# Kernel optimization log

Measured on AMD Instinct MI355X. Metric: run time of the kernel, lower is better.

The kernel has to match this reference:

```python
import jax, jax.numpy as jnp
import numpy as np

HEADS = 8
DIM_HEAD = 32
SCALE = DIM_HEAD ** (-0.5)


def setup_inputs() -> dict:
    key = jax.random.key(0)
    k1, k2, k3 = jax.random.split(key, 3)
    b, c, d, h, w = 4, 128, 32, 32, 32
    hidden = HEADS * DIM_HEAD  # 256
    x = jax.random.normal(k1, (b, c, d, h, w), dtype=jnp.float32)
    # 1x1x1 convs are channel GEMMs; store kernels as [out, in]
    w_qkv = jax.random.normal(k2, (3 * hidden, c), dtype=jnp.float32) * (1.0 / np.sqrt(c))
    w_out = jax.random.normal(k3, (c, hidden), dtype=jnp.float32) * (1.0 / np.sqrt(hidden))
    b_out = jnp.zeros((c,), dtype=jnp.float32)
    return {"x": x, "w_qkv": w_qkv, "w_out": w_out, "b_out": b_out}


def reference(x, w_qkv, w_out, b_out):
    b, c, d, h, w = x.shape
    n = d * h * w
    xf = x.reshape(b, c, n)  # [b, c, n]
    qkv = jnp.einsum('oc,bcn->bon', w_qkv, xf)  # [b, 3*hidden, n]
    q, k, v = jnp.split(qkv, 3, axis=1)
    # [b, heads, dim_head, n]
    q = q.reshape(b, HEADS, DIM_HEAD, n)
    k = k.reshape(b, HEADS, DIM_HEAD, n)
    v = v.reshape(b, HEADS, DIM_HEAD, n)
    q = jax.nn.softmax(q, axis=-2) * SCALE  # softmax over feature dim
    k = jax.nn.softmax(k, axis=-1)          # softmax over sequence dim
    context = jnp.einsum('bhdn,bhen->bhde', k, v)  # [b,h,d,e]
    out = jnp.einsum('bhde,bhdn->bhen', context, q)  # [b,h,e,n]
    out = out.reshape(b, HEADS * DIM_HEAD, n)
    out = jnp.einsum('oc,bcn->bon', w_out, out) + b_out[None, :, None]
    return out.reshape(b, c, d, h, w)
```

## Files before the change

### kernel.cpp

```cpp
#include <hip/hip_runtime.h>
#include <hip/hip_bf16.h>

#define CC 128
#define NN 32768
#define QSCALE 0.17677669529663687f

typedef unsigned short ushort_t;
typedef __attribute__((ext_vector_type(8))) short bf16x8;
typedef __attribute__((ext_vector_type(4))) short short4v;
typedef __attribute__((ext_vector_type(4))) float f32x4;

#define U_WQB    0
#define U_WKVB   32768
#define U_MFOLD  98304
#define F_PART   114688
#define F_PACC   4440064
#define F_SACC   4472832

#define XPITCH 136
#define KVP 72
#define QPITCH 264

__device__ __forceinline__ ushort_t f2b(float f) {
    __hip_bfloat16 h = __float2bfloat16(f);
    return *reinterpret_cast<ushort_t*>(&h);
}
__device__ __forceinline__ float b2f(ushort_t u) {
    union { unsigned u32; float f; } cv; cv.u32 = (unsigned)u << 16; return cv.f;
}
__device__ __forceinline__ f32x4 mfma16(bf16x8 a, bf16x8 b, f32x4 c) {
    return __builtin_amdgcn_mfma_f32_16x16x32_bf16(a, b, c, 0, 0, 0);
}

__global__ void prep_kernel(const float* __restrict__ wqkv, ushort_t* __restrict__ wsb,
                            float* __restrict__ Pacc, float* __restrict__ sacc) {
    int idx = blockIdx.x * 256 + threadIdx.x;
    if (idx < 32768) {
        wsb[U_WQB + idx] = f2b(wqkv[idx]);
        Pacc[idx] = 0.f;
        if (idx < 1024) sacc[idx] = 0.f;
    } else {
        int i2 = idx - 32768;
        int p = i2 >> 15, r = (i2 >> 7) & 255, c = i2 & 127;
        int hh = r >> 6, t = (r >> 5) & 1, d = r & 31;
        int src = 256 + t * 256 + (p * 4 + hh) * 32 + d;
        wsb[U_WKVB + i2] = f2b(wqkv[src * 128 + c]);
    }
}

__global__ __launch_bounds__(512, 4) void kv_context_kernel(
        const float* __restrict__ x, const ushort_t* __restrict__ wkvb,
        float* __restrict__ part) {
    __shared__ ushort_t u_lds[8 * 64 * KVP];
    int blk = blockIdx.x;
    int b = blk >> 7, win = blk & 127;
    int tid = threadIdx.x;
    int lane = tid & 63, wv = tid >> 6;
    int l16 = lane & 15, quad = lane >> 4;

    f32x4 accP[2][2];
    #pragma unroll
    for (int i = 0; i < 2; ++i)
        #pragma unroll
        for (int j = 0; j < 2; ++j) accP[i][j] = (f32x4){0.f, 0.f, 0.f, 0.f};
    float accSl0 = 0.f, accSl1 = 0.f;

    ushort_t* x_lds = u_lds;
    ushort_t* kvw = u_lds + wv * (64 * KVP);
    int ct = tid >> 4;
    int n4v = (tid & 15) * 4;
    int c0 = ct * 4;
    const float* xb = x + ((size_t)(b * 128 + c0)) * NN;
    const ushort_t* wbase = wkvb + wv * (64 * 128);

    #pragma unroll 1
    for (int ch = 0; ch < 4; ++ch) {
        int n0 = win * 256 + ch * 64;
        float4 r0 = *(const float4*)(xb + 0 * (size_t)NN + n0 + n4v);
        float4 r1 = *(const float4*)(xb + 1 * (size_t)NN + n0 + n4v);
        float4 r2 = *(const float4*)(xb + 2 * (size_t)NN + n0 + n4v);
        float4 r3 = *(const float4*)(xb + 3 * (size_t)NN + n0 + n4v);
        { short4v pk; pk[0]=(short)f2b(r0.x); pk[1]=(short)f2b(r1.x); pk[2]=(short)f2b(r2.x); pk[3]=(short)f2b(r3.x);
          *(short4v*)&x_lds[(n4v + 0) * XPITCH + c0] = pk; }
        { short4v pk; pk[0]=(short)f2b(r0.y); pk[1]=(short)f2b(r1.y); pk[2]=(short)f2b(r2.y); pk[3]=(short)f2b(r3.y);
          *(short4v*)&x_lds[(n4v + 1) * XPITCH + c0] = pk; }
        { short4v pk; pk[0]=(short)f2b(r0.z); pk[1]=(short)f2b(r1.z); pk[2]=(short)f2b(r2.z); pk[3]=(short)f2b(r3.z);
          *(short4v*)&x_lds[(n4v + 2) * XPITCH + c0] = pk; }
        { short4v pk; pk[0]=(short)f2b(r0.w); pk[1]=(short)f2b(r1.w); pk[2]=(short)f2b(r2.w); pk[3]=(short)f2b(r3.w);
          *(short4v*)&x_lds[(n4v + 3) * XPITCH + c0] = pk; }
        __syncthreads();
        bf16x8 xf[4][4];
        #pragma unroll
        for (int s = 0; s < 4; ++s)
            #pragma unroll
            for (int k = 0; k < 4; ++k)
                xf[s][k] = *(const bf16x8*)&x_lds[(s * 16 + l16) * XPITCH + k * 32 + quad * 8];
        __syncthreads();
        #pragma unroll
        for (int T = 0; T < 4; ++T) {
            f32x4 a0 = (f32x4){0.f,0.f,0.f,0.f}, a1 = a0, a2 = a0, a3 = a0;
            #pragma unroll
            for (int k = 0; k < 4; ++k) {
                bf16x8 wfk = *(const bf16x8*)&wbase[(T * 16 + l16) * 128 + k * 32 + quad * 8];
                a0 = mfma16(xf[0][k], wfk, a0);
                a1 = mfma16(xf[1][k], wfk, a1);
                a2 = mfma16(xf[2][k], wfk, a2);
                a3 = mfma16(xf[3][k], wfk, a3);
            }
            #pragma unroll
            for (int s = 0; s < 4; ++s) {
                f32x4 a = (s == 0) ? a0 : (s == 1) ? a1 : (s == 2) ? a2 : a3;
                short4v pk;
                if (T < 2) {
                    #pragma unroll
                    for (int r = 0; r < 4; ++r) pk[r] = (short)f2b(__expf(a[r]));
                    float es = b2f((ushort_t)pk[0]) + b2f((ushort_t)pk[1])
                             + b2f((ushort_t)pk[2]) + b2f((ushort_t)pk[3]);
                    if (T == 0) accSl0 += es; else accSl1 += es;
                } else {
                    #pragma unroll
                    for (int r = 0; r < 4; ++r) pk[r] = (short)f2b(a[r]);
                }
                *(short4v*)&kvw[(T * 16 + l16) * KVP + s * 16 + quad * 4] = pk;
            }
        }
        #pragma unroll
        for (int k2 = 0; k2 < 2; ++k2) {
            int noff = k2 * 32 + quad * 8;
            bf16x8 ea0 = *(const bf16x8*)&kvw[(0 * 16 + l16) * KVP + noff];
            bf16x8 ea1 = *(const bf16x8*)&kvw[(1 * 16 + l16) * KVP + noff];
            bf16x8 vb0 = *(const bf16x8*)&kvw[(32 + 0 * 16 + l16) * KVP + noff];
            bf16x8 vb1 = *(const bf16x8*)&kvw[(32 + 1 * 16 + l16) * KVP + noff];
            accP[0][0] = mfma16(ea0, vb0, accP[0][0]);
            accP[0][1] = mfma16(ea0, vb1, accP[0][1]);
            accP[1][0] = mfma16(ea1, vb0, accP[1][0]);
            accP[1][1] = mfma16(ea1, vb1, accP[1][1]);
        }
        __syncthreads();
    }
    float s0 = accSl0; s0 += __shfl_xor(s0, 16); s0 += __shfl_xor(s0, 32);
    float s1 = accSl1; s1 += __shfl_xor(s1, 16); s1 += __shfl_xor(s1, 32);
    float* ph = part + (size_t)blk * 8448 + wv * 1056;
    #pragma unroll
    for (int i = 0; i < 2; ++i)
        #pragma unroll
        for (int j = 0; j < 2; ++j)
            #pragma unroll
            for (int r = 0; r < 4; ++r)
                ph[(i * 16 + quad * 4 + r) * 32 + j * 16 + l16] = accP[i][j][r];
    if (quad == 0) {
        ph[1024 + l16] = s0;
        ph[1024 + 16 + l16] = s1;
    }
}

__global__ void reduce_kernel(const float* __restrict__ part,
                              float* __restrict__ Pacc, float* __restrict__ sacc) {
    int q = blockIdx.x / 132;
    int idx = (blockIdx.x - q * 132) * 256 + threadIdx.x;
    if (idx >= 32 * 1056) return;
    int bh = idx / 1056, pos = idx - bh * 1056;
    int b = bh >> 3, h = bh & 7;
    const float* pb = part + (size_t)b * 128 * 8448 + (size_t)q * 32 * 8448 + h * 1056 + pos;
    float a = 0.f;
    #pragma unroll 8
    for (int wnd = 0; wnd < 32; ++wnd)
        a += pb[(size_t)wnd * 8448];
    if (pos < 1024) atomicAdd(Pacc + (size_t)bh * 1024 + pos, a);
    else            atomicAdd(sacc + bh * 32 + (pos - 1024), a);
}

__global__ void context_proj_kernel(const float* __restrict__ wout,
                                    const float* __restrict__ Pacc,
                                    const float* __restrict__ sacc,
                                    ushort_t* __restrict__ mfold) {
    int blk = blockIdx.x;
    int b = blk >> 7, cout = blk & 127;
    int hd = threadIdx.x;
    int h = hd >> 5, d = hd & 31;
    int bh = b * 8 + h;
    float inv = 1.0f / sacc[bh * 32 + d];
    const float* Pr = Pacc + (size_t)bh * 1024 + d * 32;
    const float* wr = wout + cout * 256 + h * 32;
    float a = 0.f;
    #pragma unroll
    for (int e = 0; e < 32; ++e) a += wr[e] * Pr[e];
    mfold[((size_t)(b * 128 + cout)) * 256 + hd] = f2b(a * inv);
}

__global__ __launch_bounds__(256, 3) void q_out_kernel(
        const float* __restrict__ x, const ushort_t* __restrict__ wqb,
        const ushort_t* __restrict__ mfold, const float* __restrict__ bout,
        float* __restrict__ out) {
    __shared__ ushort_t x_lds[64 * XPITCH];
    __shared__ ushort_t qs_lds[64 * QPITCH];
    int blk = blockIdx.x;
    int b = blk >> 9, tile = blk & 511;
    int n0 = tile * 64;
    int tid = threadIdx.x;
    int lane = tid & 63, wv = tid >> 6;
    int l16 = lane & 15, quad = lane >> 4;

    const ushort_t* wq = wqb + ((wv * 64 + l16) * 128) + quad * 8;

    {
        int ct = tid >> 4, n4v = (tid & 15) * 4;
        #pragma unroll
        for (int i = 0; i < 2; ++i) {
            int c0 = i * 64 + ct * 4;
            const float* xb = x + ((size_t)(b * 128 + c0)) * NN + n0 + n4v;
            float4 r0 = *(const float4*)(xb + 0 * (size_t)NN);
            float4 r1 = *(const float4*)(xb + 1 * (size_t)NN);
            float4 r2 = *(const float4*)(xb + 2 * (size_t)NN);
            float4 r3 = *(const float4*)(xb + 3 * (size_t)NN);
            { short4v pk; pk[0]=(short)f2b(r0.x); pk[1]=(short)f2b(r1.x); pk[2]=(short)f2b(r2.x); pk[3]=(short)f2b(r3.x);
              *(short4v*)&x_lds[(n4v + 0) * XPITCH + c0] = pk; }
            { short4v pk; pk[0]=(short)f2b(r0.y); pk[1]=(short)f2b(r1.y); pk[2]=(short)f2b(r2.y); pk[3]=(short)f2b(r3.y);
              *(short4v*)&x_lds[(n4v + 1) * XPITCH + c0] = pk; }
            { short4v pk; pk[0]=(short)f2b(r0.z); pk[1]=(short)f2b(r1.z); pk[2]=(short)f2b(r2.z); pk[3]=(short)f2b(r3.z);
              *(short4v*)&x_lds[(n4v + 2) * XPITCH + c0] = pk; }
            { short4v pk; pk[0]=(short)f2b(r0.w); pk[1]=(short)f2b(r1.w); pk[2]=(short)f2b(r2.w); pk[3]=(short)f2b(r3.w);
              *(short4v*)&x_lds[(n4v + 3) * XPITCH + c0] = pk; }
        }
    }
    bf16x8 afA[4], afB[4];
    #pragma unroll
    for (int mt = 0; mt < 4; ++mt)
        afA[mt] = *(const bf16x8*)&wq[mt * 2048];
    __syncthreads();

    f32x4 acc[4][4];
    #pragma unroll
    for (int mt = 0; mt < 4; ++mt)
        #pragma unroll
        for (int nt = 0; nt < 4; ++nt) acc[mt][nt] = (f32x4){0.f, 0.f, 0.f, 0.f};
    #pragma unroll
    for (int k = 0; k < 4; ++k) {
        if (k < 3) {
            #pragma unroll
            for (int mt = 0; mt < 4; ++mt)
                afB[mt] = *(const bf16x8*)&wq[mt * 2048 + (k + 1) * 32];
        }
        bf16x8 xfk[4];
        #pragma unroll
        for (int nt = 0; nt < 4; ++nt)
            xfk[nt] = *(const bf16x8*)&x_lds[(nt * 16 + l16) * XPITCH + k * 32 + quad * 8];
        #pragma unroll
        for (int mt = 0; mt < 4; ++mt)
            #pragma unroll
            for (int nt = 0; nt < 4; ++nt)
                acc[mt][nt] = mfma16(afA[mt], xfk[nt], acc[mt][nt]);
        if (k < 3) {
            #pragma unroll
            for (int mt = 0; mt < 4; ++mt) afA[mt] = afB[mt];
        }
    }

    bf16x8 mfr[8][2];
    {
        const ushort_t* mfp = mfold + (size_t)b * 128 * 256 + (wv * 32 + l16) * 256 + quad * 8;
        #pragma unroll
        for (int k = 0; k < 8; ++k)
            #pragma unroll
            for (int mi = 0; mi < 2; ++mi)
                mfr[k][mi] = *(const bf16x8*)&mfp[mi * 16 * 256 + k * 32];
    }

    #pragma unroll
    for (int hh = 0; hh < 2; ++hh) {
        #pragma unroll
        for (int nt = 0; nt < 4; ++nt) {
            float mx = -1e30f;
            #pragma unroll
            for (int t = 0; t < 2; ++t)
                #pragma unroll
                for (int r = 0; r < 4; ++r) mx = fmaxf(mx, acc[2 * hh + t][nt][r]);
            mx = fmaxf(mx, __shfl_xor(mx, 16));
            mx = fmaxf(mx, __shfl_xor(mx, 32));
            float e[2][4], sm = 0.f;
            #pragma unroll
            for (int t = 0; t < 2; ++t)
                #pragma unroll
                for (int r = 0; r < 4; ++r) {
                    e[t][r] = __expf(acc[2 * hh + t][nt][r] - mx);
                    sm += e[t][r];
                }
            sm += __shfl_xor(sm, 16);
            sm += __shfl_xor(sm, 32);
            float sc = QSCALE / sm;
            int n = nt * 16 + l16;
            #pragma unroll
            for (int t = 0; t < 2; ++t) {
                short4v pk;
                #pragma unroll
                for (int r = 0; r < 4; ++r) pk[r] = (short)f2b(e[t][r] * sc);
                *(short4v*)&qs_lds[n * QPITCH + wv * 64 + hh * 32 + t * 16 + quad * 4] = pk;
            }
        }
    }
    __syncthreads();

    f32x4 acc2[2][4];
    #pragma unroll
    for (int mi = 0; mi < 2; ++mi)
        #pragma unroll
        for (int nt = 0; nt < 4; ++nt) acc2[mi][nt] = (f32x4){0.f, 0.f, 0.f, 0.f};
    #pragma unroll
    for (int k = 0; k < 8; ++k) {
        bf16x8 bf[4];
        #pragma unroll
        for (int nt = 0; nt < 4; ++nt)
            bf[nt] = *(const bf16x8*)&qs_lds[(nt * 16 + l16) * QPITCH + k * 32 + quad * 8];
        #pragma unroll
        for (int mi = 0; mi < 2; ++mi)
            #pragma unroll
            for (int nt = 0; nt < 4; ++nt)
                acc2[mi][nt] = mfma16(mfr[k][mi], bf[nt], acc2[mi][nt]);
    }
    float bias_r[2][4];
    #pragma unroll
    for (int mi = 0; mi < 2; ++mi)
        #pragma unroll
        for (int r = 0; r < 4; ++r)
            bias_r[mi][r] = bout[wv * 32 + mi * 16 + quad * 4 + r];
    #pragma unroll
    for (int mi = 0; mi < 2; ++mi)
        #pragma unroll
        for (int nt = 0; nt < 4; ++nt)
            #pragma unroll
            for (int r = 0; r < 4; ++r) {
                int row = wv * 32 + mi * 16 + quad * 4 + r;
                out[((size_t)(b * 128 + row)) * NN + n0 + nt * 16 + l16] =
                    acc2[mi][nt][r] + bias_r[mi][r];
            }
}

extern "C" void kernel_launch(void* const* d_in, const int* in_sizes, int n_in,
                              void* d_out, int out_size, void* d_ws, size_t ws_size,
                              hipStream_t stream) {
    (void)in_sizes; (void)n_in; (void)out_size; (void)ws_size;
    const float* x    = (const float*)d_in[0];
    const float* wqkv = (const float*)d_in[1];
    const float* wout = (const float*)d_in[2];
    const float* bout = (const float*)d_in[3];
    float* out = (float*)d_out;
    float* ws = (float*)d_ws;
    ushort_t* wsb = (ushort_t*)d_ws;

    prep_kernel<<<384, 256, 0, stream>>>(wqkv, wsb, ws + F_PACC, ws + F_SACC);
    kv_context_kernel<<<512, 512, 0, stream>>>(x, wsb + U_WKVB, ws + F_PART);
    reduce_kernel<<<528, 256, 0, stream>>>(ws + F_PART, ws + F_PACC, ws + F_SACC);
    context_proj_kernel<<<512, 256, 0, stream>>>(wout, ws + F_PACC, ws + F_SACC,
                                                 wsb + U_MFOLD);
    q_out_kernel<<<2048, 256, 0, stream>>>(x, wsb + U_WQB, wsb + U_MFOLD, bout, out);
}
```

Baseline: 216.9 us.

## Swizzle LDS layouts, prefetch x and weights, coalesce partial-context stores

Replaces the padded LDS pitches with XOR-swizzled layouts for the x tile and the per-wave k/v tiles, so the padding is gone and bank conflicts are meant to stay low. It prefetches the next x chunk into registers during compute and double-buffers the weight fragments in registers. x fragments are now read from LDS inside the MFMA loop rather than held in registers, which removes one barrier. Partial-context stores get a coalesced layout, and the reduce kernel's indexing is remapped to match. The cost is higher register pressure under launch_bounds(512,4), and more LDS reads because x fragments are re-read for each T.

```diff
diff --git a/kernel.cpp b/kernel.cpp
--- a/kernel.cpp
+++ b/kernel.cpp
@@ -18,8 +18,12 @@
 #define F_SACC   4472832
 
 #define XPITCH 136
-#define KVP 72
 #define QPITCH 264
+
+#define XP2 128
+#define KV2 64
+#define XI(n, cb) ((n) * XP2 + ((((cb)) ^ ((((n) >> 1) & 7) << 4)) >> 1))
+#define KI(r, cb) ((r) * KV2 + ((((cb)) ^ ((((r) >> 1) & 7) << 4)) >> 1))
 
 __device__ __forceinline__ ushort_t f2b(float f) {
     __hip_bfloat16 h = __float2bfloat16(f);
@@ -51,7 +55,8 @@
 __global__ __launch_bounds__(512, 4) void kv_context_kernel(
         const float* __restrict__ x, const ushort_t* __restrict__ wkvb,
         float* __restrict__ part) {
-    __shared__ ushort_t u_lds[8 * 64 * KVP];
+    __shared__ ushort_t x_lds[64 * XP2];
+    __shared__ ushort_t kv_lds[8 * 64 * KV2];
     int blk = blockIdx.x;
     int b = blk >> 7, win = blk & 127;
     int tid = threadIdx.x;
@@ -65,48 +70,61 @@
         for (int j = 0; j < 2; ++j) accP[i][j] = (f32x4){0.f, 0.f, 0.f, 0.f};
     float accSl0 = 0.f, accSl1 = 0.f;
 
-    ushort_t* x_lds = u_lds;
-    ushort_t* kvw = u_lds + wv * (64 * KVP);
+    ushort_t* kvw = kv_lds + wv * (64 * KV2);
     int ct = tid >> 4;
     int n4v = (tid & 15) * 4;
-    int c0 = ct * 4;
-    const float* xb = x + ((size_t)(b * 128 + c0)) * NN;
+    int cbw = ct * 8;
+    const float* xb = x + ((size_t)(b * 128 + ct * 4)) * NN;
     const ushort_t* wbase = wkvb + wv * (64 * 128);
+
+    float4 r0 = *(const float4*)(xb + 0 * (size_t)NN + win * 256 + n4v);
+    float4 r1 = *(const float4*)(xb + 1 * (size_t)NN + win * 256 + n4v);
+    float4 r2 = *(const float4*)(xb + 2 * (size_t)NN + win * 256 + n4v);
+    float4 r3 = *(const float4*)(xb + 3 * (size_t)NN + win * 256 + n4v);
+    bf16x8 wfA[4], wfB[4];
+    #pragma unroll
+    for (int k = 0; k < 4; ++k)
+        wfA[k] = *(const bf16x8*)&wbase[l16 * 128 + k * 32 + quad * 8];
 
     #pragma unroll 1
     for (int ch = 0; ch < 4; ++ch) {
-        int n0 = win * 256 + ch * 64;
-        float4 r0 = *(const float4*)(xb + 0 * (size_t)NN + n0 + n4v);
-        float4 r1 = *(const float4*)(xb + 1 * (size_t)NN + n0 + n4v);
-        float4 r2 = *(const float4*)(xb + 2 * (size_t)NN + n0 + n4v);
-        float4 r3 = *(const float4*)(xb + 3 * (size_t)NN + n0 + n4v);
         { short4v pk; pk[0]=(short)f2b(r0.x); pk[1]=(short)f2b(r1.x); pk[2]=(short)f2b(r2.x); pk[3]=(short)f2b(r3.x);
-          *(short4v*)&x_lds[(n4v + 0) * XPITCH + c0] = pk; }
+          *(short4v*)&x_lds[XI(n4v + 0, cbw)] = pk; }
         { short4v pk; pk[0]=(short)f2b(r0.y); pk[1]=(short)f2b(r1.y); pk[2]=(short)f2b(r2.y); pk[3]=(short)f2b(r3.y);
-          *(short4v*)&x_lds[(n4v + 1) * XPITCH + c0] = pk; }
+          *(short4v*)&x_lds[XI(n4v + 1, cbw)] = pk; }
         { short4v pk; pk[0]=(short)f2b(r0.z); pk[1]=(short)f2b(r1.z); pk[2]=(short)f2b(r2.z); pk[3]=(short)f2b(r3.z);
-          *(short4v*)&x_lds[(n4v + 2) * XPITCH + c0] = pk; }
+          *(short4v*)&x_lds[XI(n4v + 2, cbw)] = pk; }
         { short4v pk; pk[0]=(short)f2b(r0.w); pk[1]=(short)f2b(r1.w); pk[2]=(short)f2b(r2.w); pk[3]=(short)f2b(r3.w);
-          *(short4v*)&x_lds[(n4v + 3) * XPITCH + c0] = pk; }
+          *(short4v*)&x_lds[XI(n4v + 3, cbw)] = pk; }
         __syncthreads();
-        bf16x8 xf[4][4];
-        #pragma unroll
-        for (int s = 0; s < 4; ++s)
-            #pragma unroll
-            for (int k = 0; k < 4; ++k)
-                xf[s][k] = *(const bf16x8*)&x_lds[(s * 16 + l16) * XPITCH + k * 32 + quad * 8];
-        __syncthreads();
+        if (ch < 3) {
+            int n1 = win * 256 + (ch + 1) * 64;
+            r0 = *(const float4*)(xb + 0 * (size_t)NN + n1 + n4v);
+            r1 = *(const float4*)(xb + 1 * (size_t)NN + n1 + n4v);
+            r2 = *(const float4*)(xb + 2 * (size_t)NN + n1 + n4v);
+            r3 = *(const float4*)(xb + 3 * (size_t)NN + n1 + n4v);
+        }
         #pragma unroll
         for (int T = 0; T < 4; ++T) {
+            if (T < 3) {
+                #pragma unroll
+                for (int k = 0; k < 4; ++k)
+                    wfB[k] = *(const bf16x8*)&wbase[((T + 1) * 16 + l16) * 128 + k * 32 + quad * 8];
+            }
             f32x4 a0 = (f32x4){0.f,0.f,0.f,0.f}, a1 = a0, a2 = a0, a3 = a0;
             #pragma unroll
             for (int k = 0; k < 4; ++k) {
-                bf16x8 wfk = *(const bf16x8*)&wbase[(T * 16 + l16) * 128 + k * 32 + quad * 8];
-                a0 = mfma16(xf[0][k], wfk, a0);
-                a1 = mfma16(xf[1][k], wfk, a1);
-                a2 = mfma16(xf[2][k], wfk, a2);
-                a3 = mfma16(xf[3][k], wfk, a3);
-            }
+                int cb = k * 64 + quad * 16;
+                bf16x8 x0 = *(const bf16x8*)&x_lds[XI( 0 + l16, cb)];
+                bf16x8 x1 = *(const bf16x8*)&x_lds[XI(16 + l16, cb)];
+                bf16x8 x2 = *(const bf16x8*)&x_lds[XI(32 + l16, cb)];
+                bf16x8 x3 = *(const bf16x8*)&x_lds[XI(48 + l16, cb)];
+                a0 = mfma16(x0, wfA[k], a0);
+                a1 = mfma16(x1, wfA[k], a1);
+                a2 = mfma16(x2, wfA[k], a2);
+                a3 = mfma16(x3, wfA[k], a3);
+            }
+            int row = T * 16 + l16;
             #pragma unroll
             for (int s = 0; s < 4; ++s) {
                 f32x4 a = (s == 0) ? a0 : (s == 1) ? a1 : (s == 2) ? a2 : a3;
@@ -121,21 +139,30 @@
                     #pragma unroll
                     for (int r = 0; r < 4; ++r) pk[r] = (short)f2b(a[r]);
                 }
-                *(short4v*)&kvw[(T * 16 + l16) * KVP + s * 16 + quad * 4] = pk;
+                *(short4v*)&kvw[KI(row, s * 32 + quad * 8)] = pk;
+            }
+            if (T < 3) {
+                #pragma unroll
+                for (int k = 0; k < 4; ++k) wfA[k] = wfB[k];
             }
         }
         #pragma unroll
         for (int k2 = 0; k2 < 2; ++k2) {
-            int noff = k2 * 32 + quad * 8;
-            bf16x8 ea0 = *(const bf16x8*)&kvw[(0 * 16 + l16) * KVP + noff];
-            bf16x8 ea1 = *(const bf16x8*)&kvw[(1 * 16 + l16) * KVP + noff];
-            bf16x8 vb0 = *(const bf16x8*)&kvw[(32 + 0 * 16 + l16) * KVP + noff];
-            bf16x8 vb1 = *(const bf16x8*)&kvw[(32 + 1 * 16 + l16) * KVP + noff];
+            int cb = k2 * 64 + quad * 16;
+            bf16x8 ea0 = *(const bf16x8*)&kvw[KI( 0 + l16, cb)];
+            bf16x8 ea1 = *(const bf16x8*)&kvw[KI(16 + l16, cb)];
+            bf16x8 vb0 = *(const bf16x8*)&kvw[KI(32 + l16, cb)];
+            bf16x8 vb1 = *(const bf16x8*)&kvw[KI(48 + l16, cb)];
             accP[0][0] = mfma16(ea0, vb0, accP[0][0]);
             accP[0][1] = mfma16(ea0, vb1, accP[0][1]);
             accP[1][0] = mfma16(ea1, vb0, accP[1][0]);
             accP[1][1] = mfma16(ea1, vb1, accP[1][1]);
         }
+        if (ch < 3) {
+            #pragma unroll
+            for (int k = 0; k < 4; ++k)
+                wfA[k] = *(const bf16x8*)&wbase[l16 * 128 + k * 32 + quad * 8];
+        }
         __syncthreads();
     }
     float s0 = accSl0; s0 += __shfl_xor(s0, 16); s0 += __shfl_xor(s0, 32);
@@ -147,7 +174,7 @@
         for (int j = 0; j < 2; ++j)
             #pragma unroll
             for (int r = 0; r < 4; ++r)
-                ph[(i * 16 + quad * 4 + r) * 32 + j * 16 + l16] = accP[i][j][r];
+                ph[((i * 2 + j) * 4 + r) * 64 + quad * 16 + l16] = accP[i][j][r];
     if (quad == 0) {
         ph[1024 + l16] = s0;
         ph[1024 + 16 + l16] = s1;
@@ -161,7 +188,16 @@
     if (idx >= 32 * 1056) return;
     int bh = idx / 1056, pos = idx - bh * 1056;
     int b = bh >> 3, h = bh & 7;
-    const float* pb = part + (size_t)b * 128 * 8448 + (size_t)q * 32 * 8448 + h * 1056 + pos;
+    int f;
+    if (pos < 1024) {
+        int d = pos >> 5, e = pos & 31;
+        int i = d >> 4, qd = (d >> 2) & 3, r = d & 3;
+        int j = e >> 4, l = e & 15;
+        f = ((i * 2 + j) * 4 + r) * 64 + qd * 16 + l;
+    } else {
+        f = pos;
+    }
+    const float* pb = part + (size_t)b * 128 * 8448 + (size_t)q * 32 * 8448 + h * 1056 + f;
     float a = 0.f;
     #pragma unroll 8
     for (int wnd = 0; wnd < 32; ++wnd)
```

After: 276.1 us. 1.27x slower.
